# Optimization experiments

Measured on AMD Instinct MI355X. Metric: run time of the kernel, lower is better.

## Reference

```python
import jax, jax.numpy as jnp
import numpy as np

N, D, H, Y = 2048, 768, 12, 64


def setup_inputs() -> dict:
    key = jax.random.key(0)
    kg, kq, kk = jax.random.split(key, 3)
    g = jax.random.normal(kg, (N, D), dtype=jnp.float32)
    Wq = jax.random.normal(kq, (H, Y, D), dtype=jnp.float32)
    Wk = jax.random.normal(kk, (H, Y, D), dtype=jnp.float32)
    return {"g": g, "Wq": Wq, "Wk": Wk}


def reference(g, Wq, Wk):
    # g: [N, D]; Wq, Wk: [H, Y, D]
    beta = 1.0 / jnp.sqrt(jnp.asarray(Y, dtype=g.dtype))
    K = jnp.einsum('kd,hzd->khz', g, Wk)          # [N, H, Y]
    Q = jnp.einsum('qd,hzd->qhz', g, Wq)          # [N, H, Y]
    scores = beta * jnp.einsum('qhz,khz->hqk', Q, K)  # [H, N, N]
    A = jax.nn.logsumexp(scores, axis=-1)         # [H, N]
    return (-1.0 / beta) * A.sum()
```

## Files before the change

### kernel.cpp

```cpp
#include <hip/hip_runtime.h>
#include <hip/hip_bf16.h>

#define NN 2048
#define DD 768
#define HH 12
#define HW 1536
#define SPLITS 4
#define KPW (NN/SPLITS)
#define NCH (KPW/64)

typedef __attribute__((ext_vector_type(8))) short bf16x8;
typedef __attribute__((ext_vector_type(4))) float f32x4;

__device__ __forceinline__ float exp2g(float x) { return __builtin_amdgcn_exp2f(x); }
__device__ __forceinline__ float log2g(float x) { return __builtin_amdgcn_logf(x); }

#define QSCALE 0.18033688011112042f

__device__ __forceinline__ unsigned short bfbits(float x) {
  __hip_bfloat16 h = __float2bfloat16(x);
  return *reinterpret_cast<unsigned short*>(&h);
}

__device__ __forceinline__ void cvt_store(__hip_bfloat16* dst, float4 a, float4 b, float sc) {
  union { uint4 v; unsigned short s[8]; } u;
  u.s[0] = bfbits(a.x * sc); u.s[1] = bfbits(a.y * sc);
  u.s[2] = bfbits(a.z * sc); u.s[3] = bfbits(a.w * sc);
  u.s[4] = bfbits(b.x * sc); u.s[5] = bfbits(b.y * sc);
  u.s[6] = bfbits(b.z * sc); u.s[7] = bfbits(b.w * sc);
  *reinterpret_cast<uint4*>(dst) = u.v;
}

#define LDP 72
__global__ __launch_bounds__(256) void proj_kernel(
    const float* __restrict__ g, const float* __restrict__ Wq,
    const float* __restrict__ Wk, __hip_bfloat16* __restrict__ QK,
    float* __restrict__ out) {
  __shared__ __align__(16) __hip_bfloat16 As[2][64 * LDP];
  __shared__ __align__(16) __hip_bfloat16 Bs[2][64 * LDP];
  if (blockIdx.x == 0 && blockIdx.y == 0 && threadIdx.x == 0) out[0] = 0.0f;
  const int t = threadIdx.x;
  const int wave = t >> 6, lane = t & 63;
  const int lr = lane & 15, lg = lane >> 4;
  const int wm = wave & 1, wn = wave >> 1;
  const int bm = blockIdx.x, bn = blockIdx.y;
  const int r0 = t >> 3, s0 = (t & 7) * 8;
  const int r1 = (t + 256) >> 3;

  const float bscale = (bn < HH) ? QSCALE : 1.0f;
  const float* wsrc = (bn < HH) ? Wq : Wk;
  const int wrow = (bn < HH) ? bn * 64 : (bn - HH) * 64;

  const float* ga0 = g + (bm * 64 + r0) * DD + s0;
  const float* ga1 = g + (bm * 64 + r1) * DD + s0;
  const float* gb0 = wsrc + (wrow + r0) * DD + s0;
  const float* gb1 = wsrc + (wrow + r1) * DD + s0;

  f32x4 acc[2][2] = {};

  {
    float4 a0 = *reinterpret_cast<const float4*>(ga0);
    float4 a0h = *reinterpret_cast<const float4*>(ga0 + 4);
    float4 a1 = *reinterpret_cast<const float4*>(ga1);
    float4 a1h = *reinterpret_cast<const float4*>(ga1 + 4);
    float4 b0 = *reinterpret_cast<const float4*>(gb0);
    float4 b0h = *reinterpret_cast<const float4*>(gb0 + 4);
    float4 b1 = *reinterpret_cast<const float4*>(gb1);
    float4 b1h = *reinterpret_cast<const float4*>(gb1 + 4);
    cvt_store(&As[0][r0 * LDP + s0], a0, a0h, 1.0f);
    cvt_store(&As[0][r1 * LDP + s0], a1, a1h, 1.0f);
    cvt_store(&Bs[0][r0 * LDP + s0], b0, b0h, bscale);
    cvt_store(&Bs[0][r1 * LDP + s0], b1, b1h, bscale);
  }
  __syncthreads();

  for (int it = 0; it < 12; ++it) {
    const int cur = it & 1;
    float4 na0, na0h, na1, na1h, nb0, nb0h, nb1, nb1h;
    if (it < 11) {
      const int kt = (it + 1) * 64;
      na0 = *reinterpret_cast<const float4*>(ga0 + kt);
      na0h = *reinterpret_cast<const float4*>(ga0 + kt + 4);
      na1 = *reinterpret_cast<const float4*>(ga1 + kt);
      na1h = *reinterpret_cast<const float4*>(ga1 + kt + 4);
      nb0 = *reinterpret_cast<const float4*>(gb0 + kt);
      nb0h = *reinterpret_cast<const float4*>(gb0 + kt + 4);
      nb1 = *reinterpret_cast<const float4*>(gb1 + kt);
      nb1h = *reinterpret_cast<const float4*>(gb1 + kt + 4);
    }
#pragma unroll
    for (int ks = 0; ks < 2; ++ks) {
      bf16x8 a[2], b[2];
#pragma unroll
      for (int mt = 0; mt < 2; ++mt)
        a[mt] = *reinterpret_cast<const bf16x8*>(&As[cur][(wm * 32 + mt * 16 + lr) * LDP + ks * 32 + lg * 8]);
#pragma unroll
      for (int nt = 0; nt < 2; ++nt)
        b[nt] = *reinterpret_cast<const bf16x8*>(&Bs[cur][(wn * 32 + nt * 16 + lr) * LDP + ks * 32 + lg * 8]);
#pragma unroll
      for (int mt = 0; mt < 2; ++mt)
#pragma unroll
        for (int nt = 0; nt < 2; ++nt)
          acc[mt][nt] = __builtin_amdgcn_mfma_f32_16x16x32_bf16(a[mt], b[nt], acc[mt][nt], 0, 0, 0);
    }
    if (it < 11) {
      cvt_store(&As[cur ^ 1][r0 * LDP + s0], na0, na0h, 1.0f);
      cvt_store(&As[cur ^ 1][r1 * LDP + s0], na1, na1h, 1.0f);
      cvt_store(&Bs[cur ^ 1][r0 * LDP + s0], nb0, nb0h, bscale);
      cvt_store(&Bs[cur ^ 1][r1 * LDP + s0], nb1, nb1h, bscale);
      __syncthreads();
    }
  }
#pragma unroll
  for (int mt = 0; mt < 2; ++mt) {
    int row = bm * 64 + wm * 32 + mt * 16 + lg * 4;
#pragma unroll
    for (int nt = 0; nt < 2; ++nt) {
      int col = bn * 64 + wn * 32 + nt * 16 + lr;
#pragma unroll
      for (int r = 0; r < 4; ++r)
        QK[(row + r) * HW + col] = __float2bfloat16(acc[mt][nt][r]);
    }
  }
}

#define LDA 72
__global__ __launch_bounds__(256) void attn_kernel(
    const __hip_bfloat16* __restrict__ QK, float2* __restrict__ part) {
  __shared__ __align__(16) __hip_bfloat16 Ks[2][64 * LDA];
  const int t = threadIdx.x;
  const int wave = t >> 6, lane = t & 63;
  const int lr = lane & 15, lg = lane >> 4;
  const int q0 = blockIdx.x * 128, h = blockIdx.y, sp = blockIdx.z;
  const int k0 = sp * KPW;
  const int r0 = t >> 3, s0 = (t & 7) * 8;
  const int r1 = (t + 256) >> 3, s1 = s0;
  const int colK = DD + h * 64;

  bf16x8 aq[2][2];
#pragma unroll
  for (int mt = 0; mt < 2; ++mt)
#pragma unroll
    for (int z = 0; z < 2; ++z)
      aq[mt][z] = *reinterpret_cast<const bf16x8*>(
          QK + (q0 + wave * 32 + mt * 16 + lr) * HW + h * 64 + z * 32 + lg * 8);

  *reinterpret_cast<uint4*>(&Ks[0][r0 * LDA + s0]) =
      *reinterpret_cast<const uint4*>(QK + (k0 + r0) * HW + colK + s0);
  *reinterpret_cast<uint4*>(&Ks[0][r1 * LDA + s1]) =
      *reinterpret_cast<const uint4*>(QK + (k0 + r1) * HW + colK + s1);
  __syncthreads();

  float m[2][4], l[2][4];
#pragma unroll
  for (int mt = 0; mt < 2; ++mt)
#pragma unroll
    for (int r = 0; r < 4; ++r) { m[mt][r] = -3.0e38f; l[mt][r] = 0.0f; }

  for (int ci = 0; ci < NCH; ++ci) {
    const int cur = ci & 1;
    uint4 n0, n1;
    if (ci < NCH - 1) {
      int kc = k0 + (ci + 1) * 64;
      n0 = *reinterpret_cast<const uint4*>(QK + (kc + r0) * HW + colK + s0);
      n1 = *reinterpret_cast<const uint4*>(QK + (kc + r1) * HW + colK + s1);
    }
    bf16x8 b[4][2];
#pragma unroll
    for (int nt = 0; nt < 4; ++nt)
#pragma unroll
      for (int z = 0; z < 2; ++z)
        b[nt][z] = *reinterpret_cast<const bf16x8*>(&Ks[cur][(nt * 16 + lr) * LDA + z * 32 + lg * 8]);

    f32x4 s[2][4] = {};
#pragma unroll
    for (int mt = 0; mt < 2; ++mt)
#pragma unroll
      for (int nt = 0; nt < 4; ++nt)
#pragma unroll
        for (int z = 0; z < 2; ++z)
          s[mt][nt] = __builtin_amdgcn_mfma_f32_16x16x32_bf16(aq[mt][z], b[nt][z], s[mt][nt], 0, 0, 0);

#pragma unroll
    for (int mt = 0; mt < 2; ++mt)
#pragma unroll
      for (int r = 0; r < 4; ++r) {
        float v0 = s[mt][0][r], v1 = s[mt][1][r], v2 = s[mt][2][r], v3 = s[mt][3][r];
        float cm = fmaxf(fmaxf(v0, v1), fmaxf(v2, v3));
        float mn = fmaxf(m[mt][r], cm);
        float p = exp2g(v0 - mn) + exp2g(v1 - mn) +
                  exp2g(v2 - mn) + exp2g(v3 - mn);
        l[mt][r] = l[mt][r] * exp2g(m[mt][r] - mn) + p;
        m[mt][r] = mn;
      }
    if (ci < NCH - 1) {
      *reinterpret_cast<uint4*>(&Ks[cur ^ 1][r0 * LDA + s0]) = n0;
      *reinterpret_cast<uint4*>(&Ks[cur ^ 1][r1 * LDA + s1]) = n1;
      __syncthreads();
    }
  }
#pragma unroll
  for (int msk = 1; msk <= 8; msk <<= 1) {
#pragma unroll
    for (int mt = 0; mt < 2; ++mt)
#pragma unroll
      for (int r = 0; r < 4; ++r) {
        float mo = __shfl_xor(m[mt][r], msk);
        float lo = __shfl_xor(l[mt][r], msk);
        float mn = fmaxf(m[mt][r], mo);
        l[mt][r] = l[mt][r] * exp2g(m[mt][r] - mn) + lo * exp2g(mo - mn);
        m[mt][r] = mn;
      }
  }
  if (lr == 0) {
#pragma unroll
    for (int mt = 0; mt < 2; ++mt)
#pragma unroll
      for (int r = 0; r < 4; ++r) {
        int q = q0 + wave * 32 + mt * 16 + lg * 4 + r;
        part[(sp * HH + h) * NN + q] = make_float2(m[mt][r], l[mt][r]);
      }
  }
}

__global__ __launch_bounds__(1024) void reduce_kernel(
    const float2* __restrict__ part, float* __restrict__ out) {
  const int t = threadIdx.x;
  const int row = blockIdx.x * 1024 + t;
  float2 p0 = part[row];
  float2 p1 = part[24576 + row];
  float2 p2 = part[49152 + row];
  float2 p3 = part[73728 + row];
  float mm = fmaxf(fmaxf(p0.x, p1.x), fmaxf(p2.x, p3.x));
  float ll = p0.y * exp2g(p0.x - mm) + p1.y * exp2g(p1.x - mm) +
             p2.y * exp2g(p2.x - mm) + p3.y * exp2g(p3.x - mm);
  float lse = mm + log2g(ll);
#pragma unroll
  for (int msk = 1; msk <= 32; msk <<= 1)
    lse += __shfl_xor(lse, msk);
  __shared__ float wsum[16];
  if ((t & 63) == 0) wsum[t >> 6] = lse;
  __syncthreads();
  if (t == 0) {
    float s = 0.0f;
#pragma unroll
    for (int i = 0; i < 16; ++i) s += wsum[i];
    atomicAdd(out, -5.545177444479562f * s);
  }
}

extern "C" void kernel_launch(void* const* d_in, const int* in_sizes, int n_in,
                              void* d_out, int out_size, void* d_ws, size_t ws_size,
                              hipStream_t stream) {
  const float* g  = (const float*)d_in[0];
  const float* Wq = (const float*)d_in[1];
  const float* Wk = (const float*)d_in[2];
  float* out = (float*)d_out;

  __hip_bfloat16* QK = (__hip_bfloat16*)d_ws;
  float2* part = (float2*)((char*)d_ws + (size_t)NN * HW * 2);

  proj_kernel<<<dim3(32, 24), 256, 0, stream>>>(g, Wq, Wk, QK, out);
  attn_kernel<<<dim3(16, HH, SPLITS), 256, 0, stream>>>(QK, part);
  reduce_kernel<<<24, 1024, 0, stream>>>(part, out);
}
```

Baseline: 96.89 us.

## Fuse final LSE reduction into attention kernel via atomic ticket

Removes the separate reduce kernel launch. The last 24 attention blocks to finish (by atomic ticket order) spin until all blocks have arrived, then each combines a slice of the split partials and atomically accumulates into the output. The Q scaling also moves from the per-element bf16 conversion of Wq to the epilogue of the projection GEMM. This saves one launch and the gap between kernels, at the cost of spin-waiting blocks and a change in Q rounding order.

```diff
diff --git a/kernel.cpp b/kernel.cpp
--- a/kernel.cpp
+++ b/kernel.cpp
@@ -8,6 +8,9 @@
 #define SPLITS 4
 #define KPW (NN/SPLITS)
 #define NCH (KPW/64)
+#define NBLK (16*HH*SPLITS)
+#define NROWS (HH*NN)
+#define FINB 24
 
 typedef __attribute__((ext_vector_type(8))) short bf16x8;
 typedef __attribute__((ext_vector_type(4))) float f32x4;
@@ -22,12 +25,12 @@
   return *reinterpret_cast<unsigned short*>(&h);
 }
 
-__device__ __forceinline__ void cvt_store(__hip_bfloat16* dst, float4 a, float4 b, float sc) {
+__device__ __forceinline__ void cvt_store(__hip_bfloat16* dst, float4 a, float4 b) {
   union { uint4 v; unsigned short s[8]; } u;
-  u.s[0] = bfbits(a.x * sc); u.s[1] = bfbits(a.y * sc);
-  u.s[2] = bfbits(a.z * sc); u.s[3] = bfbits(a.w * sc);
-  u.s[4] = bfbits(b.x * sc); u.s[5] = bfbits(b.y * sc);
-  u.s[6] = bfbits(b.z * sc); u.s[7] = bfbits(b.w * sc);
+  u.s[0] = bfbits(a.x); u.s[1] = bfbits(a.y);
+  u.s[2] = bfbits(a.z); u.s[3] = bfbits(a.w);
+  u.s[4] = bfbits(b.x); u.s[5] = bfbits(b.y);
+  u.s[6] = bfbits(b.z); u.s[7] = bfbits(b.w);
   *reinterpret_cast<uint4*>(dst) = u.v;
 }
 
@@ -35,10 +38,13 @@
 __global__ __launch_bounds__(256) void proj_kernel(
     const float* __restrict__ g, const float* __restrict__ Wq,
     const float* __restrict__ Wk, __hip_bfloat16* __restrict__ QK,
-    float* __restrict__ out) {
+    float* __restrict__ out, unsigned int* __restrict__ ticket) {
   __shared__ __align__(16) __hip_bfloat16 As[2][64 * LDP];
   __shared__ __align__(16) __hip_bfloat16 Bs[2][64 * LDP];
-  if (blockIdx.x == 0 && blockIdx.y == 0 && threadIdx.x == 0) out[0] = 0.0f;
+  if (blockIdx.x == 0 && blockIdx.y == 0 && threadIdx.x == 0) {
+    out[0] = 0.0f;
+    *ticket = 0u;
+  }
   const int t = threadIdx.x;
   const int wave = t >> 6, lane = t & 63;
   const int lr = lane & 15, lg = lane >> 4;
@@ -47,9 +53,9 @@
   const int r0 = t >> 3, s0 = (t & 7) * 8;
   const int r1 = (t + 256) >> 3;
 
-  const float bscale = (bn < HH) ? QSCALE : 1.0f;
   const float* wsrc = (bn < HH) ? Wq : Wk;
   const int wrow = (bn < HH) ? bn * 64 : (bn - HH) * 64;
+  const float oscale = (bn < HH) ? QSCALE : 1.0f;
 
   const float* ga0 = g + (bm * 64 + r0) * DD + s0;
   const float* ga1 = g + (bm * 64 + r1) * DD + s0;
@@ -67,10 +73,10 @@
     float4 b0h = *reinterpret_cast<const float4*>(gb0 + 4);
     float4 b1 = *reinterpret_cast<const float4*>(gb1);
     float4 b1h = *reinterpret_cast<const float4*>(gb1 + 4);
-    cvt_store(&As[0][r0 * LDP + s0], a0, a0h, 1.0f);
-    cvt_store(&As[0][r1 * LDP + s0], a1, a1h, 1.0f);
-    cvt_store(&Bs[0][r0 * LDP + s0], b0, b0h, bscale);
-    cvt_store(&Bs[0][r1 * LDP + s0], b1, b1h, bscale);
+    cvt_store(&As[0][r0 * LDP + s0], a0, a0h);
+    cvt_store(&As[0][r1 * LDP + s0], a1, a1h);
+    cvt_store(&Bs[0][r0 * LDP + s0], b0, b0h);
+    cvt_store(&Bs[0][r1 * LDP + s0], b1, b1h);
   }
   __syncthreads();
 
@@ -104,10 +110,10 @@
           acc[mt][nt] = __builtin_amdgcn_mfma_f32_16x16x32_bf16(a[mt], b[nt], acc[mt][nt], 0, 0, 0);
     }
     if (it < 11) {
-      cvt_store(&As[cur ^ 1][r0 * LDP + s0], na0, na0h, 1.0f);
-      cvt_store(&As[cur ^ 1][r1 * LDP + s0], na1, na1h, 1.0f);
-      cvt_store(&Bs[cur ^ 1][r0 * LDP + s0], nb0, nb0h, bscale);
-      cvt_store(&Bs[cur ^ 1][r1 * LDP + s0], nb1, nb1h, bscale);
+      cvt_store(&As[cur ^ 1][r0 * LDP + s0], na0, na0h);
+      cvt_store(&As[cur ^ 1][r1 * LDP + s0], na1, na1h);
+      cvt_store(&Bs[cur ^ 1][r0 * LDP + s0], nb0, nb0h);
+      cvt_store(&Bs[cur ^ 1][r1 * LDP + s0], nb1, nb1h);
       __syncthreads();
     }
   }
@@ -119,15 +125,18 @@
       int col = bn * 64 + wn * 32 + nt * 16 + lr;
 #pragma unroll
       for (int r = 0; r < 4; ++r)
-        QK[(row + r) * HW + col] = __float2bfloat16(acc[mt][nt][r]);
+        QK[(row + r) * HW + col] = __float2bfloat16(acc[mt][nt][r] * oscale);
     }
   }
 }
 
 #define LDA 72
 __global__ __launch_bounds__(256) void attn_kernel(
-    const __hip_bfloat16* __restrict__ QK, float2* __restrict__ part) {
+    const __hip_bfloat16* __restrict__ QK, float2* __restrict__ part,
+    float* __restrict__ out, unsigned int* __restrict__ ticket) {
   __shared__ __align__(16) __hip_bfloat16 Ks[2][64 * LDA];
+  __shared__ unsigned int s_old;
+  __shared__ float wsum[4];
   const int t = threadIdx.x;
   const int wave = t >> 6, lane = t & 63;
   const int lr = lane & 15, lg = lane >> 4;
@@ -221,31 +230,41 @@
         part[(sp * HH + h) * NN + q] = make_float2(m[mt][r], l[mt][r]);
       }
   }
-}
-
-__global__ __launch_bounds__(1024) void reduce_kernel(
-    const float2* __restrict__ part, float* __restrict__ out) {
-  const int t = threadIdx.x;
-  const int row = blockIdx.x * 1024 + t;
-  float2 p0 = part[row];
-  float2 p1 = part[24576 + row];
-  float2 p2 = part[49152 + row];
-  float2 p3 = part[73728 + row];
-  float mm = fmaxf(fmaxf(p0.x, p1.x), fmaxf(p2.x, p3.x));
-  float ll = p0.y * exp2g(p0.x - mm) + p1.y * exp2g(p1.x - mm) +
-             p2.y * exp2g(p2.x - mm) + p3.y * exp2g(p3.x - mm);
-  float lse = mm + log2g(ll);
-#pragma unroll
-  for (int msk = 1; msk <= 32; msk <<= 1)
-    lse += __shfl_xor(lse, msk);
-  __shared__ float wsum[16];
-  if ((t & 63) == 0) wsum[t >> 6] = lse;
+
   __syncthreads();
   if (t == 0) {
-    float s = 0.0f;
-#pragma unroll
-    for (int i = 0; i < 16; ++i) s += wsum[i];
-    atomicAdd(out, -5.545177444479562f * s);
+    __threadfence();
+    s_old = atomicAdd(ticket, 1u);
+  }
+  __syncthreads();
+  const unsigned int old = s_old;
+  if (old >= (unsigned)(NBLK - FINB) && old < (unsigned)NBLK) {
+    if (t == 0) {
+      while (atomicAdd(ticket, 0u) < (unsigned)NBLK) __builtin_amdgcn_s_sleep(8);
+    }
+    __syncthreads();
+    __threadfence();
+    const int base = (int)(old - (unsigned)(NBLK - FINB)) * 1024;
+    float lsum = 0.0f;
+#pragma unroll
+    for (int i = 0; i < 4; ++i) {
+      int row = base + i * 256 + t;
+      float2 p0 = part[row];
+      float2 p1 = part[NROWS + row];
+      float2 p2 = part[2 * NROWS + row];
+      float2 p3 = part[3 * NROWS + row];
+      float mm = fmaxf(fmaxf(p0.x, p1.x), fmaxf(p2.x, p3.x));
+      float ll = p0.y * exp2g(p0.x - mm) + p1.y * exp2g(p1.x - mm) +
+                 p2.y * exp2g(p2.x - mm) + p3.y * exp2g(p3.x - mm);
+      lsum += mm + log2g(ll);
+    }
+#pragma unroll
+    for (int msk = 1; msk <= 32; msk <<= 1)
+      lsum += __shfl_xor(lsum, msk);
+    if (lane == 0) wsum[wave] = lsum;
+    __syncthreads();
+    if (t == 0)
+      atomicAdd(out, -5.545177444479562f * (wsum[0] + wsum[1] + wsum[2] + wsum[3]));
   }
 }
 
@@ -259,8 +278,9 @@
 
   __hip_bfloat16* QK = (__hip_bfloat16*)d_ws;
   float2* part = (float2*)((char*)d_ws + (size_t)NN * HW * 2);
-
-  proj_kernel<<<dim3(32, 24), 256, 0, stream>>>(g, Wq, Wk, QK, out);
-  attn_kernel<<<dim3(16, HH, SPLITS), 256, 0, stream>>>(QK, part);
-  reduce_kernel<<<24, 1024, 0, stream>>>(part, out);
-}
+  unsigned int* ticket = (unsigned int*)((char*)d_ws + (size_t)NN * HW * 2
+                                         + (size_t)SPLITS * NROWS * sizeof(float2));
+
+  proj_kernel<<<dim3(32, 24), 256, 0, stream>>>(g, Wq, Wk, QK, out, ticket);
+  attn_kernel<<<dim3(16, HH, SPLITS), 256, 0, stream>>>(QK, part, out, ticket);
+}
```

After: 118.5 us. 22.3% more time.

## Enlarge projection GEMM M-tile to 128 and swizzle block order

Applied to the files above, without the earlier changes.

The projection GEMM now computes a 128x64 output tile per block instead of 64x64, doubling per-wave MFMA work and halving the number of re-reads of the weight tiles. A 1D grid with a bijective swizzle maps blocks so that neighbouring blocks share g or W tiles, aiming for better L2 reuse. The Q scaling by QSCALE moves from the bf16 conversion of W to the fp32 accumulator at store, which changes rounding slightly. The grid shrinks from 768 to 384 blocks, which may lower occupancy on a 256-CU device and raises register and LDS use.

```diff
diff --git a/kernel.cpp b/kernel.cpp
--- a/kernel.cpp
+++ b/kernel.cpp
@@ -8,6 +8,7 @@
 #define SPLITS 4
 #define KPW (NN/SPLITS)
 #define NCH (KPW/64)
+#define NROWS (HH*NN)
 
 typedef __attribute__((ext_vector_type(8))) short bf16x8;
 typedef __attribute__((ext_vector_type(4))) float f32x4;
@@ -22,12 +23,12 @@
   return *reinterpret_cast<unsigned short*>(&h);
 }
 
-__device__ __forceinline__ void cvt_store(__hip_bfloat16* dst, float4 a, float4 b, float sc) {
+__device__ __forceinline__ void cvt_store(__hip_bfloat16* dst, float4 a, float4 b) {
   union { uint4 v; unsigned short s[8]; } u;
-  u.s[0] = bfbits(a.x * sc); u.s[1] = bfbits(a.y * sc);
-  u.s[2] = bfbits(a.z * sc); u.s[3] = bfbits(a.w * sc);
-  u.s[4] = bfbits(b.x * sc); u.s[5] = bfbits(b.y * sc);
-  u.s[6] = bfbits(b.z * sc); u.s[7] = bfbits(b.w * sc);
+  u.s[0] = bfbits(a.x); u.s[1] = bfbits(a.y);
+  u.s[2] = bfbits(a.z); u.s[3] = bfbits(a.w);
+  u.s[4] = bfbits(b.x); u.s[5] = bfbits(b.y);
+  u.s[6] = bfbits(b.z); u.s[7] = bfbits(b.w);
   *reinterpret_cast<uint4*>(dst) = u.v;
 }
 
@@ -36,90 +37,93 @@
     const float* __restrict__ g, const float* __restrict__ Wq,
     const float* __restrict__ Wk, __hip_bfloat16* __restrict__ QK,
     float* __restrict__ out) {
-  __shared__ __align__(16) __hip_bfloat16 As[2][64 * LDP];
+  __shared__ __align__(16) __hip_bfloat16 As[2][128 * LDP];
   __shared__ __align__(16) __hip_bfloat16 Bs[2][64 * LDP];
-  if (blockIdx.x == 0 && blockIdx.y == 0 && threadIdx.x == 0) out[0] = 0.0f;
+  if (blockIdx.x == 0 && threadIdx.x == 0) out[0] = 0.0f;
   const int t = threadIdx.x;
   const int wave = t >> 6, lane = t & 63;
   const int lr = lane & 15, lg = lane >> 4;
   const int wm = wave & 1, wn = wave >> 1;
-  const int bm = blockIdx.x, bn = blockIdx.y;
-  const int r0 = t >> 3, s0 = (t & 7) * 8;
-  const int r1 = (t + 256) >> 3;
-
-  const float bscale = (bn < HH) ? QSCALE : 1.0f;
+  const int bid = blockIdx.x;
+  const int swz = (bid & 7) * 48 + (bid >> 3);
+  const int bm = swz / 24, bn = swz % 24;
+  const int rr = t >> 3, ss = (t & 7) * 8;
+
   const float* wsrc = (bn < HH) ? Wq : Wk;
   const int wrow = (bn < HH) ? bn * 64 : (bn - HH) * 64;
-
-  const float* ga0 = g + (bm * 64 + r0) * DD + s0;
-  const float* ga1 = g + (bm * 64 + r1) * DD + s0;
-  const float* gb0 = wsrc + (wrow + r0) * DD + s0;
-  const float* gb1 = wsrc + (wrow + r1) * DD + s0;
-
-  f32x4 acc[2][2] = {};
+  const float oscale = (bn < HH) ? QSCALE : 1.0f;
+
+  const float* ga = g + (bm * 128 + rr) * DD + ss;
+  const float* gb = wsrc + (wrow + rr) * DD + ss;
+
+  f32x4 acc[4][2] = {};
 
   {
-    float4 a0 = *reinterpret_cast<const float4*>(ga0);
-    float4 a0h = *reinterpret_cast<const float4*>(ga0 + 4);
-    float4 a1 = *reinterpret_cast<const float4*>(ga1);
-    float4 a1h = *reinterpret_cast<const float4*>(ga1 + 4);
-    float4 b0 = *reinterpret_cast<const float4*>(gb0);
-    float4 b0h = *reinterpret_cast<const float4*>(gb0 + 4);
-    float4 b1 = *reinterpret_cast<const float4*>(gb1);
-    float4 b1h = *reinterpret_cast<const float4*>(gb1 + 4);
-    cvt_store(&As[0][r0 * LDP + s0], a0, a0h, 1.0f);
-    cvt_store(&As[0][r1 * LDP + s0], a1, a1h, 1.0f);
-    cvt_store(&Bs[0][r0 * LDP + s0], b0, b0h, bscale);
-    cvt_store(&Bs[0][r1 * LDP + s0], b1, b1h, bscale);
+#pragma unroll
+    for (int u = 0; u < 4; ++u) {
+      float4 lo = *reinterpret_cast<const float4*>(ga + u * 32 * DD);
+      float4 hi = *reinterpret_cast<const float4*>(ga + u * 32 * DD + 4);
+      cvt_store(&As[0][(rr + u * 32) * LDP + ss], lo, hi);
+    }
+#pragma unroll
+    for (int u = 0; u < 2; ++u) {
+      float4 lo = *reinterpret_cast<const float4*>(gb + u * 32 * DD);
+      float4 hi = *reinterpret_cast<const float4*>(gb + u * 32 * DD + 4);
+      cvt_store(&Bs[0][(rr + u * 32) * LDP + ss], lo, hi);
+    }
   }
   __syncthreads();
 
   for (int it = 0; it < 12; ++it) {
     const int cur = it & 1;
-    float4 na0, na0h, na1, na1h, nb0, nb0h, nb1, nb1h;
+    float4 nal[4], nah[4], nbl[2], nbh[2];
     if (it < 11) {
       const int kt = (it + 1) * 64;
-      na0 = *reinterpret_cast<const float4*>(ga0 + kt);
-      na0h = *reinterpret_cast<const float4*>(ga0 + kt + 4);
-      na1 = *reinterpret_cast<const float4*>(ga1 + kt);
-      na1h = *reinterpret_cast<const float4*>(ga1 + kt + 4);
-      nb0 = *reinterpret_cast<const float4*>(gb0 + kt);
-      nb0h = *reinterpret_cast<const float4*>(gb0 + kt + 4);
-      nb1 = *reinterpret_cast<const float4*>(gb1 + kt);
-      nb1h = *reinterpret_cast<const float4*>(gb1 + kt + 4);
+#pragma unroll
+      for (int u = 0; u < 4; ++u) {
+        nal[u] = *reinterpret_cast<const float4*>(ga + u * 32 * DD + kt);
+        nah[u] = *reinterpret_cast<const float4*>(ga + u * 32 * DD + kt + 4);
+      }
+#pragma unroll
+      for (int u = 0; u < 2; ++u) {
+        nbl[u] = *reinterpret_cast<const float4*>(gb + u * 32 * DD + kt);
+        nbh[u] = *reinterpret_cast<const float4*>(gb + u * 32 * DD + kt + 4);
+      }
     }
 #pragma unroll
     for (int ks = 0; ks < 2; ++ks) {
-      bf16x8 a[2], b[2];
-#pragma unroll
-      for (int mt = 0; mt < 2; ++mt)
-        a[mt] = *reinterpret_cast<const bf16x8*>(&As[cur][(wm * 32 + mt * 16 + lr) * LDP + ks * 32 + lg * 8]);
+      bf16x8 a[4], b[2];
+#pragma unroll
+      for (int mt = 0; mt < 4; ++mt)
+        a[mt] = *reinterpret_cast<const bf16x8*>(&As[cur][(wm * 64 + mt * 16 + lr) * LDP + ks * 32 + lg * 8]);
 #pragma unroll
       for (int nt = 0; nt < 2; ++nt)
         b[nt] = *reinterpret_cast<const bf16x8*>(&Bs[cur][(wn * 32 + nt * 16 + lr) * LDP + ks * 32 + lg * 8]);
 #pragma unroll
-      for (int mt = 0; mt < 2; ++mt)
+      for (int mt = 0; mt < 4; ++mt)
 #pragma unroll
         for (int nt = 0; nt < 2; ++nt)
           acc[mt][nt] = __builtin_amdgcn_mfma_f32_16x16x32_bf16(a[mt], b[nt], acc[mt][nt], 0, 0, 0);
     }
     if (it < 11) {
-      cvt_store(&As[cur ^ 1][r0 * LDP + s0], na0, na0h, 1.0f);
-      cvt_store(&As[cur ^ 1][r1 * LDP + s0], na1, na1h, 1.0f);
-      cvt_store(&Bs[cur ^ 1][r0 * LDP + s0], nb0, nb0h, bscale);
-      cvt_store(&Bs[cur ^ 1][r1 * LDP + s0], nb1, nb1h, bscale);
+#pragma unroll
+      for (int u = 0; u < 4; ++u)
+        cvt_store(&As[cur ^ 1][(rr + u * 32) * LDP + ss], nal[u], nah[u]);
+#pragma unroll
+      for (int u = 0; u < 2; ++u)
+        cvt_store(&Bs[cur ^ 1][(rr + u * 32) * LDP + ss], nbl[u], nbh[u]);
       __syncthreads();
     }
   }
 #pragma unroll
-  for (int mt = 0; mt < 2; ++mt) {
-    int row = bm * 64 + wm * 32 + mt * 16 + lg * 4;
+  for (int mt = 0; mt < 4; ++mt) {
+    int row = bm * 128 + wm * 64 + mt * 16 + lg * 4;
 #pragma unroll
     for (int nt = 0; nt < 2; ++nt) {
       int col = bn * 64 + wn * 32 + nt * 16 + lr;
 #pragma unroll
       for (int r = 0; r < 4; ++r)
-        QK[(row + r) * HW + col] = __float2bfloat16(acc[mt][nt][r]);
+        QK[(row + r) * HW + col] = __float2bfloat16(acc[mt][nt][r] * oscale);
     }
   }
 }
@@ -228,9 +232,9 @@
   const int t = threadIdx.x;
   const int row = blockIdx.x * 1024 + t;
   float2 p0 = part[row];
-  float2 p1 = part[24576 + row];
-  float2 p2 = part[49152 + row];
-  float2 p3 = part[73728 + row];
+  float2 p1 = part[NROWS + row];
+  float2 p2 = part[2 * NROWS + row];
+  float2 p3 = part[3 * NROWS + row];
   float mm = fmaxf(fmaxf(p0.x, p1.x), fmaxf(p2.x, p3.x));
   float ll = p0.y * exp2g(p0.x - mm) + p1.y * exp2g(p1.x - mm) +
              p2.y * exp2g(p2.x - mm) + p3.y * exp2g(p3.x - mm);
@@ -260,7 +264,7 @@
   __hip_bfloat16* QK = (__hip_bfloat16*)d_ws;
   float2* part = (float2*)((char*)d_ws + (size_t)NN * HW * 2);
 
-  proj_kernel<<<dim3(32, 24), 256, 0, stream>>>(g, Wq, Wk, QK, out);
+  proj_kernel<<<384, 256, 0, stream>>>(g, Wq, Wk, QK, out);
   attn_kernel<<<dim3(16, HH, SPLITS), 256, 0, stream>>>(QK, part);
   reduce_kernel<<<24, 1024, 0, stream>>>(part, out);
 }
```

Result: no change. 95.82 us (median of 2 runs) (-1.1%).
